# Kernel optimization log

Measured on AMD Instinct MI355X. Metric: run time of the kernel, lower is better.

The kernel has to match this reference:

```python
import jax, jax.numpy as jnp
import numpy as np

DIM = 96
NUM_HEADS = 3
WIN = 7  # window_size (square)


def _relative_position_index(wh, ww):
    coords = np.stack(np.meshgrid(np.arange(wh), np.arange(ww), indexing='ij'))  # [2, wh, ww]
    flat = coords.reshape(2, -1)  # [2, n]
    rel = flat[:, :, None] - flat[:, None, :]  # [2, n, n]
    rel = rel.transpose(1, 2, 0).astype(np.int64)
    rel[..., 0] += wh - 1
    rel[..., 1] += ww - 1
    rel[..., 0] *= 2 * ww - 1
    return rel.sum(-1)  # [n, n]


def setup_inputs() -> dict:
    key = jax.random.key(0)
    ks = jax.random.split(key, 9)
    b, n, c = 8192, WIN * WIN, DIM
    std = 0.02
    inp = {
        'x': jax.random.normal(ks[0], (b, n, c), jnp.float32),
        'v': jax.random.normal(ks[1], (b, n, c), jnp.float32),
        'w_q': jax.random.normal(ks[2], (c, c), jnp.float32) * std,
        'b_q': jnp.zeros((c,), jnp.float32),
        'w_kv': jax.random.normal(ks[3], (c, 2 * c), jnp.float32) * std,
        'b_kv': jnp.zeros((2 * c,), jnp.float32),
        'w_proj': jax.random.normal(ks[4], (c, c), jnp.float32) * std,
        'b_proj': jnp.zeros((c,), jnp.float32),
        'rpb_table': jax.random.normal(ks[5], ((2 * WIN - 1) * (2 * WIN - 1), NUM_HEADS), jnp.float32) * std,
        'rel_index': jnp.asarray(_relative_position_index(WIN, WIN), jnp.int32),
    }
    return inp


def reference(x, v, w_q, b_q, w_kv, b_kv, w_proj, b_proj, rpb_table, rel_index):
    b, n, c = x.shape
    h = NUM_HEADS
    hd = c // h
    scale = hd ** -0.5
    # q: [b, h, n, hd]
    q = (x @ w_q + b_q).reshape(b, n, h, hd).transpose(0, 2, 1, 3) * scale
    kv = (v @ w_kv + b_kv).reshape(b, n, 2, h, hd)
    k = kv[:, :, 0].transpose(0, 2, 1, 3)  # [b, h, n, hd]
    vv = kv[:, :, 1].transpose(0, 2, 1, 3)
    attn = jnp.einsum('bhqd,bhkd->bhqk', q, k)  # [b, h, n, n]
    bias = rpb_table[rel_index.reshape(-1)].reshape(n, n, h).transpose(2, 0, 1)  # [h, n, n]
    attn = jax.nn.softmax(attn + bias[None], axis=-1)
    out = jnp.einsum('bhqk,bhkd->bhqd', attn, vv).transpose(0, 2, 1, 3).reshape(b, n, c)
    return out @ w_proj + b_proj
```

## Files before the change

### kernel.cpp

```cpp
#include <hip/hip_runtime.h>
#include <hip/hip_bf16.h>

typedef __bf16 bf16x8 __attribute__((ext_vector_type(8)));
typedef float f32x4 __attribute__((ext_vector_type(4)));
typedef short s16x8 __attribute__((ext_vector_type(8)));
typedef short s16x4 __attribute__((ext_vector_type(4)));

#define NTOK 49
#define CDIM 96
#define XS_S 104
#define VT_S 72
#define PW_S 72

__device__ __forceinline__ unsigned short f2bf(float f) {
  __hip_bfloat16 h = __float2bfloat16(f);
  return __builtin_bit_cast(unsigned short, h);
}

__global__ void prep(const float* __restrict__ wq, const float* __restrict__ wkv,
                     const float* __restrict__ wproj, const float* __restrict__ rpb,
                     const int* __restrict__ relidx, unsigned short* __restrict__ wsT,
                     float* __restrict__ biasf) {
  const int total = 36864 + 3 * 49 * 64;
  for (int i = blockIdx.x * 256 + threadIdx.x; i < total; i += gridDim.x * 256) {
    if (i < 9216) {
      int oc = i / 96, ic = i - oc * 96;
      wsT[i] = f2bf(wq[ic * 96 + oc]);
    } else if (i < 27648) {
      int j = i - 9216; int oc = j / 96, ic = j - oc * 96;
      wsT[i] = f2bf(wkv[ic * 192 + oc]);
    } else if (i < 36864) {
      int j = i - 27648; int oc = j / 96, ic = j - oc * 96;
      wsT[i] = f2bf(wproj[ic * 96 + oc]);
    } else {
      int j = i - 36864; int h = j / 3136; int rc = j - h * 3136;
      int r = rc >> 6, c = rc & 63;
      biasf[j] = (c < 49) ? rpb[relidx[r * 49 + c] * 3 + h] : 0.f;
    }
  }
}

__launch_bounds__(256, 3)
__global__ void attn_fused(const float* __restrict__ xg, const float* __restrict__ vg,
                           const float* __restrict__ bq, const float* __restrict__ bkv,
                           const float* __restrict__ bproj,
                           const unsigned short* __restrict__ wsT,
                           const float* __restrict__ biasf,
                           float* __restrict__ outg) {
  __shared__ __align__(16) unsigned char smem[53664];
  unsigned short* Qs = (unsigned short*)(smem);
  unsigned short* Ks = (unsigned short*)(smem + 10240);
  unsigned short* Pw = (unsigned short*)(smem + 20432);
  unsigned short* XV = (unsigned short*)(smem + 29648);
  unsigned short* Vs = (unsigned short*)(smem + 43472);

  const int tid = threadIdx.x;
  const int lane = tid & 63;
  const int wv = tid >> 6;
  const int c16 = lane & 15;
  const int g4 = lane >> 4;
  const int win = blockIdx.x;
  const float* xw = xg + (size_t)win * (NTOK * CDIM);
  const float* vw = vg + (size_t)win * (NTOK * CDIM);
  const int MST[4] = {0, 16, 32, 33};

  for (int i = tid; i < 2 * 1176; i += 256) {
    int which = i >= 1176;
    int j = which ? i - 1176 : i;
    int r = j / 24, c4 = (j - r * 24) * 4;
    const float* src = which ? vw : xw;
    float4 f = *(const float4*)(src + r * 96 + c4);
    s16x4 p;
    p[0] = (short)f2bf(f.x); p[1] = (short)f2bf(f.y);
    p[2] = (short)f2bf(f.z); p[3] = (short)f2bf(f.w);
    *(s16x4*)((which ? Vs : XV) + r * XS_S + c4) = p;
  }
  __syncthreads();

  bf16x8 axf[4][3];
#pragma unroll
  for (int m = 0; m < 4; ++m)
#pragma unroll
    for (int k = 0; k < 3; ++k)
      axf[m][k] = *(const bf16x8*)(XV + (MST[m] + c16) * XS_S + k * 32 + g4 * 8);
  __syncthreads();

  unsigned short* VVT = XV;

  const float scale = 0.17677669529663687f;
  for (int nt = wv; nt < 18; nt += 4) {
    f32x4 acc[4] = {{0,0,0,0},{0,0,0,0},{0,0,0,0},{0,0,0,0}};
    const bool isq = nt < 6;
    const unsigned short* wbase = isq ? wsT : wsT + 9216;
    const int ocl = (isq ? nt * 16 : (nt - 6) * 16) + c16;
#pragma unroll
    for (int k = 0; k < 3; ++k) {
      bf16x8 b = *(const bf16x8*)(wbase + ocl * 96 + k * 32 + g4 * 8);
      if (isq) {
#pragma unroll
        for (int m = 0; m < 4; ++m)
          acc[m] = __builtin_amdgcn_mfma_f32_16x16x32_bf16(axf[m][k], b, acc[m], 0, 0, 0);
      } else {
#pragma unroll
        for (int m = 0; m < 4; ++m) {
          bf16x8 av = *(const bf16x8*)(Vs + (MST[m] + c16) * XS_S + k * 32 + g4 * 8);
          acc[m] = __builtin_amdgcn_mfma_f32_16x16x32_bf16(av, b, acc[m], 0, 0, 0);
        }
      }
    }
    if (isq) {
      float bias = bq[ocl];
#pragma unroll
      for (int m = 0; m < 4; ++m) {
        int rb = MST[m] + g4 * 4;
#pragma unroll
        for (int r = 0; r < 4; ++r)
          Qs[(rb + r) * XS_S + ocl] = f2bf((acc[m][r] + bias) * scale);
      }
    } else if (nt < 12) {
      float bias = bkv[ocl];
#pragma unroll
      for (int m = 0; m < 4; ++m) {
        int rb = MST[m] + g4 * 4;
#pragma unroll
        for (int r = 0; r < 4; ++r)
          Ks[(rb + r) * XS_S + ocl] = f2bf(acc[m][r] + bias);
      }
    } else {
      float bias = bkv[ocl];
      int dim = ocl - 96;
#pragma unroll
      for (int m = 0; m < 4; ++m) {
        int rb = MST[m] + g4 * 4;
        if (m < 3) {
          s16x4 p;
#pragma unroll
          for (int r = 0; r < 4; ++r) p[r] = (short)f2bf(acc[m][r] + bias);
          *(s16x4*)(VVT + dim * VT_S + rb) = p;
        } else {
#pragma unroll
          for (int r = 0; r < 4; ++r)
            VVT[dim * VT_S + rb + r] = f2bf(acc[m][r] + bias);
        }
      }
    }
  }
  __syncthreads();

  const int q0 = MST[wv];
  unsigned short* mypw = Pw + wv * 16 * PW_S;
  unsigned short* OUTs = Vs;

  s16x8 vmask;
#pragma unroll
  for (int j = 0; j < 8; ++j)
    vmask[j] = (short)(((32 + g4 * 8 + j) < 49) ? 0xFFFF : 0x0000);

  for (int h = 0; h < 3; ++h) {
    bf16x8 bqf = *(const bf16x8*)(Qs + (q0 + c16) * XS_S + h * 32 + g4 * 8);
    f32x4 s[4];
#pragma unroll
    for (int kt = 0; kt < 4; ++kt) {
      bf16x8 ak = *(const bf16x8*)(Ks + (16 * kt + c16) * XS_S + h * 32 + g4 * 8);
      s[kt] = __builtin_amdgcn_mfma_f32_16x16x32_bf16(ak, bqf, (f32x4){0,0,0,0}, 0, 0, 0);
    }
    const int q = q0 + c16;
    const float* brow = biasf + (h * 49 + q) * 64 + 4 * g4;
    float vals[16];
    float mx = -1e30f;
#pragma unroll
    for (int kt = 0; kt < 4; ++kt) {
      f32x4 bv = *(const f32x4*)(brow + 16 * kt);
#pragma unroll
      for (int r = 0; r < 4; ++r) {
        int key = 16 * kt + 4 * g4 + r;
        float vl = (kt < 3 || key < 49) ? (s[kt][r] + bv[r]) : -1e30f;
        vals[kt * 4 + r] = vl;
        mx = fmaxf(mx, vl);
      }
    }
    mx = fmaxf(mx, __shfl_xor(mx, 16, 64));
    mx = fmaxf(mx, __shfl_xor(mx, 32, 64));
    float sum = 0.f;
#pragma unroll
    for (int j = 0; j < 16; ++j) { vals[j] = __expf(vals[j] - mx); sum += vals[j]; }
    sum += __shfl_xor(sum, 16, 64);
    sum += __shfl_xor(sum, 32, 64);
    float rinv = 1.0f / sum;
#pragma unroll
    for (int kt = 0; kt < 4; ++kt) {
      s16x4 p;
#pragma unroll
      for (int r = 0; r < 4; ++r) p[r] = (short)f2bf(vals[kt * 4 + r] * rinv);
      *(s16x4*)(mypw + c16 * PW_S + 16 * kt + 4 * g4) = p;
    }
    asm volatile("s_waitcnt lgkmcnt(0)" ::: "memory");
    bf16x8 ap0 = *(const bf16x8*)(mypw + c16 * PW_S + g4 * 8);
    bf16x8 ap1 = *(const bf16x8*)(mypw + c16 * PW_S + 32 + g4 * 8);
#pragma unroll
    for (int dt = 0; dt < 2; ++dt) {
      int dim = h * 32 + dt * 16 + c16;
      bf16x8 bv0 = *(const bf16x8*)(VVT + dim * VT_S + g4 * 8);
      s16x8 b1 = *(const s16x8*)(VVT + dim * VT_S + 32 + g4 * 8);
      b1 &= vmask;
      f32x4 o = __builtin_amdgcn_mfma_f32_16x16x32_bf16(ap0, bv0, (f32x4){0,0,0,0}, 0, 0, 0);
      o = __builtin_amdgcn_mfma_f32_16x16x32_bf16(ap1, __builtin_bit_cast(bf16x8, b1), o, 0, 0, 0);
#pragma unroll
      for (int r = 0; r < 4; ++r)
        OUTs[(q0 + 4 * g4 + r) * XS_S + dim] = f2bf(o[r]);
    }
  }
  __syncthreads();

  {
    const int nstart = MST[wv];
    bf16x8 bo[3];
#pragma unroll
    for (int k = 0; k < 3; ++k)
      bo[k] = *(const bf16x8*)(OUTs + (nstart + c16) * XS_S + k * 32 + g4 * 8);
    const unsigned short* wp = wsT + 27648;
    const bool store_ok = (wv < 3) || (c16 == 15);
    const int token = nstart + c16;
    float* orow = outg + (size_t)win * (NTOK * CDIM) + token * 96;
#pragma unroll
    for (int mt = 0; mt < 6; ++mt) {
      f32x4 acc = {0, 0, 0, 0};
      int mrow = mt * 16 + c16;
#pragma unroll
      for (int k = 0; k < 3; ++k) {
        bf16x8 a = *(const bf16x8*)(wp + mrow * 96 + k * 32 + g4 * 8);
        acc = __builtin_amdgcn_mfma_f32_16x16x32_bf16(a, bo[k], acc, 0, 0, 0);
      }
      int oc0 = mt * 16 + g4 * 4;
      if (store_ok) {
        float4 bb = *(const float4*)(bproj + oc0);
        float4 o4;
        o4.x = acc[0] + bb.x; o4.y = acc[1] + bb.y;
        o4.z = acc[2] + bb.z; o4.w = acc[3] + bb.w;
        *(float4*)(orow + oc0) = o4;
      }
    }
  }
}

extern "C" void kernel_launch(void* const* d_in, const int* in_sizes, int n_in,
                              void* d_out, int out_size, void* d_ws, size_t ws_size,
                              hipStream_t stream) {
  const float* x     = (const float*)d_in[0];
  const float* v     = (const float*)d_in[1];
  const float* wq    = (const float*)d_in[2];
  const float* bq    = (const float*)d_in[3];
  const float* wkv   = (const float*)d_in[4];
  const float* bkv   = (const float*)d_in[5];
  const float* wproj = (const float*)d_in[6];
  const float* bproj = (const float*)d_in[7];
  const float* rpb   = (const float*)d_in[8];
  const int*   relidx= (const int*)d_in[9];
  float* out = (float*)d_out;
  unsigned short* wsT = (unsigned short*)d_ws;
  float* biasf = (float*)((char*)d_ws + 73728);
  int nwin = in_sizes[0] / (NTOK * CDIM);

  hipLaunchKernelGGL(prep, dim3(181), dim3(256), 0, stream,
                     wq, wkv, wproj, rpb, relidx, wsT, biasf);
  hipLaunchKernelGGL(attn_fused, dim3(nwin), dim3(256), 0, stream,
                     x, v, bq, bkv, bproj, wsT, biasf, out);
}
```

Baseline: 277.0 us.

## Load x/v directly to registers, fuse proj per head, shrink LDS for occupancy

Each wave now loads its own 16 token rows of x and v straight from global memory into bf16 MFMA fragments, so the LDS staging copy and two barriers go away. The Q projection stays per wave in a private buffer, and only K and V-transposed are shared. The output projection is accumulated per head inside the attention loop, so the block-wide OUTs buffer and the final barrier are no longer needed. LDS drops from about 53.7KB to 37.3KB and launch bounds rise to 4 blocks per CU. In exchange, each wave computes full-width weight tiles and rereads all 18 weight tiles from global memory, and the 6 extra accumulators raise register pressure.

```diff
diff --git a/kernel.cpp b/kernel.cpp
--- a/kernel.cpp
+++ b/kernel.cpp
@@ -8,13 +8,24 @@
 
 #define NTOK 49
 #define CDIM 96
-#define XS_S 104
+#define KS_S 104
 #define VT_S 72
-#define PW_S 72
+#define BN_S 104
 
 __device__ __forceinline__ unsigned short f2bf(float f) {
   __hip_bfloat16 h = __float2bfloat16(f);
   return __builtin_bit_cast(unsigned short, h);
+}
+
+__device__ __forceinline__ bf16x8 ld_cvt8(const float* p) {
+  float4 a = *(const float4*)p;
+  float4 b = *(const float4*)(p + 4);
+  s16x8 r;
+  r[0] = (short)f2bf(a.x); r[1] = (short)f2bf(a.y);
+  r[2] = (short)f2bf(a.z); r[3] = (short)f2bf(a.w);
+  r[4] = (short)f2bf(b.x); r[5] = (short)f2bf(b.y);
+  r[6] = (short)f2bf(b.z); r[7] = (short)f2bf(b.w);
+  return __builtin_bit_cast(bf16x8, r);
 }
 
 __global__ void prep(const float* __restrict__ wq, const float* __restrict__ wkv,
@@ -40,19 +51,16 @@
   }
 }
 
-__launch_bounds__(256, 3)
+__launch_bounds__(256, 4)
 __global__ void attn_fused(const float* __restrict__ xg, const float* __restrict__ vg,
                            const float* __restrict__ bq, const float* __restrict__ bkv,
                            const float* __restrict__ bproj,
                            const unsigned short* __restrict__ wsT,
                            const float* __restrict__ biasf,
                            float* __restrict__ outg) {
-  __shared__ __align__(16) unsigned char smem[53664];
-  unsigned short* Qs = (unsigned short*)(smem);
-  unsigned short* Ks = (unsigned short*)(smem + 10240);
-  unsigned short* Pw = (unsigned short*)(smem + 20432);
-  unsigned short* XV = (unsigned short*)(smem + 29648);
-  unsigned short* Vs = (unsigned short*)(smem + 43472);
+  __shared__ __align__(16) unsigned char smem[37328];
+  unsigned short* Ks  = (unsigned short*)smem;
+  unsigned short* VVT = (unsigned short*)(smem + 10192);
 
   const int tid = threadIdx.x;
   const int lane = tid & 63;
@@ -60,109 +68,83 @@
   const int c16 = lane & 15;
   const int g4 = lane >> 4;
   const int win = blockIdx.x;
-  const float* xw = xg + (size_t)win * (NTOK * CDIM);
-  const float* vw = vg + (size_t)win * (NTOK * CDIM);
-  const int MST[4] = {0, 16, 32, 33};
-
-  for (int i = tid; i < 2 * 1176; i += 256) {
-    int which = i >= 1176;
-    int j = which ? i - 1176 : i;
-    int r = j / 24, c4 = (j - r * 24) * 4;
-    const float* src = which ? vw : xw;
-    float4 f = *(const float4*)(src + r * 96 + c4);
-    s16x4 p;
-    p[0] = (short)f2bf(f.x); p[1] = (short)f2bf(f.y);
-    p[2] = (short)f2bf(f.z); p[3] = (short)f2bf(f.w);
-    *(s16x4*)((which ? Vs : XV) + r * XS_S + c4) = p;
+  const int q0 = (wv == 0) ? 0 : (wv == 1) ? 16 : (wv == 2) ? 32 : 33;
+  unsigned short* bnc = (unsigned short*)(smem + 24016) + wv * (16 * BN_S);
+
+  const float* xrow = xg + (size_t)win * (NTOK * CDIM) + (q0 + c16) * CDIM;
+  const float* vrow = vg + (size_t)win * (NTOK * CDIM) + (q0 + c16) * CDIM;
+
+  bf16x8 xf[3];
+#pragma unroll
+  for (int k = 0; k < 3; ++k) xf[k] = ld_cvt8(xrow + k * 32 + g4 * 8);
+  const float scale = 0.17677669529663687f;
+#pragma unroll
+  for (int nt = 0; nt < 6; ++nt) {
+    f32x4 acc = {0, 0, 0, 0};
+    const int ocl = nt * 16 + c16;
+#pragma unroll
+    for (int k = 0; k < 3; ++k) {
+      bf16x8 b = *(const bf16x8*)(wsT + ocl * 96 + k * 32 + g4 * 8);
+      acc = __builtin_amdgcn_mfma_f32_16x16x32_bf16(xf[k], b, acc, 0, 0, 0);
+    }
+    float bias = bq[ocl];
+#pragma unroll
+    for (int r = 0; r < 4; ++r)
+      bnc[(4 * g4 + r) * BN_S + ocl] = f2bf((acc[r] + bias) * scale);
+  }
+
+  bf16x8 vf[3];
+#pragma unroll
+  for (int k = 0; k < 3; ++k) vf[k] = ld_cvt8(vrow + k * 32 + g4 * 8);
+#pragma unroll
+  for (int nt = 0; nt < 12; ++nt) {
+    f32x4 acc = {0, 0, 0, 0};
+    const int ocl = nt * 16 + c16;
+#pragma unroll
+    for (int k = 0; k < 3; ++k) {
+      bf16x8 b = *(const bf16x8*)(wsT + 9216 + ocl * 96 + k * 32 + g4 * 8);
+      acc = __builtin_amdgcn_mfma_f32_16x16x32_bf16(vf[k], b, acc, 0, 0, 0);
+    }
+    float bias = bkv[ocl];
+    if (nt < 6) {
+#pragma unroll
+      for (int r = 0; r < 4; ++r)
+        Ks[(q0 + 4 * g4 + r) * KS_S + ocl] = f2bf(acc[r] + bias);
+    } else {
+      int dim = ocl - 96;
+      int rb = q0 + 4 * g4;
+      if (wv < 3) {
+        s16x4 p;
+#pragma unroll
+        for (int r = 0; r < 4; ++r) p[r] = (short)f2bf(acc[r] + bias);
+        *(s16x4*)(VVT + dim * VT_S + rb) = p;
+      } else {
+#pragma unroll
+        for (int r = 0; r < 4; ++r)
+          VVT[dim * VT_S + rb + r] = f2bf(acc[r] + bias);
+      }
+    }
   }
   __syncthreads();
 
-  bf16x8 axf[4][3];
-#pragma unroll
-  for (int m = 0; m < 4; ++m)
-#pragma unroll
-    for (int k = 0; k < 3; ++k)
-      axf[m][k] = *(const bf16x8*)(XV + (MST[m] + c16) * XS_S + k * 32 + g4 * 8);
-  __syncthreads();
-
-  unsigned short* VVT = XV;
-
-  const float scale = 0.17677669529663687f;
-  for (int nt = wv; nt < 18; nt += 4) {
-    f32x4 acc[4] = {{0,0,0,0},{0,0,0,0},{0,0,0,0},{0,0,0,0}};
-    const bool isq = nt < 6;
-    const unsigned short* wbase = isq ? wsT : wsT + 9216;
-    const int ocl = (isq ? nt * 16 : (nt - 6) * 16) + c16;
-#pragma unroll
-    for (int k = 0; k < 3; ++k) {
-      bf16x8 b = *(const bf16x8*)(wbase + ocl * 96 + k * 32 + g4 * 8);
-      if (isq) {
-#pragma unroll
-        for (int m = 0; m < 4; ++m)
-          acc[m] = __builtin_amdgcn_mfma_f32_16x16x32_bf16(axf[m][k], b, acc[m], 0, 0, 0);
-      } else {
-#pragma unroll
-        for (int m = 0; m < 4; ++m) {
-          bf16x8 av = *(const bf16x8*)(Vs + (MST[m] + c16) * XS_S + k * 32 + g4 * 8);
-          acc[m] = __builtin_amdgcn_mfma_f32_16x16x32_bf16(av, b, acc[m], 0, 0, 0);
-        }
-      }
-    }
-    if (isq) {
-      float bias = bq[ocl];
-#pragma unroll
-      for (int m = 0; m < 4; ++m) {
-        int rb = MST[m] + g4 * 4;
-#pragma unroll
-        for (int r = 0; r < 4; ++r)
-          Qs[(rb + r) * XS_S + ocl] = f2bf((acc[m][r] + bias) * scale);
-      }
-    } else if (nt < 12) {
-      float bias = bkv[ocl];
-#pragma unroll
-      for (int m = 0; m < 4; ++m) {
-        int rb = MST[m] + g4 * 4;
-#pragma unroll
-        for (int r = 0; r < 4; ++r)
-          Ks[(rb + r) * XS_S + ocl] = f2bf(acc[m][r] + bias);
-      }
-    } else {
-      float bias = bkv[ocl];
-      int dim = ocl - 96;
-#pragma unroll
-      for (int m = 0; m < 4; ++m) {
-        int rb = MST[m] + g4 * 4;
-        if (m < 3) {
-          s16x4 p;
-#pragma unroll
-          for (int r = 0; r < 4; ++r) p[r] = (short)f2bf(acc[m][r] + bias);
-          *(s16x4*)(VVT + dim * VT_S + rb) = p;
-        } else {
-#pragma unroll
-          for (int r = 0; r < 4; ++r)
-            VVT[dim * VT_S + rb + r] = f2bf(acc[m][r] + bias);
-        }
-      }
-    }
-  }
-  __syncthreads();
-
-  const int q0 = MST[wv];
-  unsigned short* mypw = Pw + wv * 16 * PW_S;
-  unsigned short* OUTs = Vs;
+  bf16x8 qf[3];
+#pragma unroll
+  for (int h = 0; h < 3; ++h)
+    qf[h] = *(const bf16x8*)(bnc + c16 * BN_S + h * 32 + g4 * 8);
 
   s16x8 vmask;
 #pragma unroll
   for (int j = 0; j < 8; ++j)
     vmask[j] = (short)(((32 + g4 * 8 + j) < 49) ? 0xFFFF : 0x0000);
 
+  f32x4 oacc[6] = {{0,0,0,0},{0,0,0,0},{0,0,0,0},{0,0,0,0},{0,0,0,0},{0,0,0,0}};
+
   for (int h = 0; h < 3; ++h) {
-    bf16x8 bqf = *(const bf16x8*)(Qs + (q0 + c16) * XS_S + h * 32 + g4 * 8);
     f32x4 s[4];
 #pragma unroll
     for (int kt = 0; kt < 4; ++kt) {
-      bf16x8 ak = *(const bf16x8*)(Ks + (16 * kt + c16) * XS_S + h * 32 + g4 * 8);
-      s[kt] = __builtin_amdgcn_mfma_f32_16x16x32_bf16(ak, bqf, (f32x4){0,0,0,0}, 0, 0, 0);
+      bf16x8 ak = *(const bf16x8*)(Ks + (16 * kt + c16) * KS_S + h * 32 + g4 * 8);
+      s[kt] = __builtin_amdgcn_mfma_f32_16x16x32_bf16(ak, qf[h], (f32x4){0,0,0,0}, 0, 0, 0);
     }
     const int q = q0 + c16;
     const float* brow = biasf + (h * 49 + q) * 64 + 4 * g4;
@@ -192,11 +174,12 @@
       s16x4 p;
 #pragma unroll
       for (int r = 0; r < 4; ++r) p[r] = (short)f2bf(vals[kt * 4 + r] * rinv);
-      *(s16x4*)(mypw + c16 * PW_S + 16 * kt + 4 * g4) = p;
+      *(s16x4*)(bnc + c16 * BN_S + 16 * kt + 4 * g4) = p;
     }
     asm volatile("s_waitcnt lgkmcnt(0)" ::: "memory");
-    bf16x8 ap0 = *(const bf16x8*)(mypw + c16 * PW_S + g4 * 8);
-    bf16x8 ap1 = *(const bf16x8*)(mypw + c16 * PW_S + 32 + g4 * 8);
+    __builtin_amdgcn_sched_barrier(0);
+    bf16x8 ap0 = *(const bf16x8*)(bnc + c16 * BN_S + g4 * 8);
+    bf16x8 ap1 = *(const bf16x8*)(bnc + c16 * BN_S + 32 + g4 * 8);
 #pragma unroll
     for (int dt = 0; dt < 2; ++dt) {
       int dim = h * 32 + dt * 16 + c16;
@@ -207,36 +190,32 @@
       o = __builtin_amdgcn_mfma_f32_16x16x32_bf16(ap1, __builtin_bit_cast(bf16x8, b1), o, 0, 0, 0);
 #pragma unroll
       for (int r = 0; r < 4; ++r)
-        OUTs[(q0 + 4 * g4 + r) * XS_S + dim] = f2bf(o[r]);
-    }
-  }
-  __syncthreads();
+        bnc[(4 * g4 + r) * BN_S + dt * 16 + c16] = f2bf(o[r]);
+    }
+    asm volatile("s_waitcnt lgkmcnt(0)" ::: "memory");
+    __builtin_amdgcn_sched_barrier(0);
+    bf16x8 bo = *(const bf16x8*)(bnc + c16 * BN_S + g4 * 8);
+#pragma unroll
+    for (int mt = 0; mt < 6; ++mt) {
+      bf16x8 a = *(const bf16x8*)(wsT + 27648 + (mt * 16 + c16) * 96 + h * 32 + g4 * 8);
+      oacc[mt] = __builtin_amdgcn_mfma_f32_16x16x32_bf16(a, bo, oacc[mt], 0, 0, 0);
+    }
+    asm volatile("s_waitcnt lgkmcnt(0)" ::: "memory");
+    __builtin_amdgcn_sched_barrier(0);
+  }
 
   {
-    const int nstart = MST[wv];
-    bf16x8 bo[3];
-#pragma unroll
-    for (int k = 0; k < 3; ++k)
-      bo[k] = *(const bf16x8*)(OUTs + (nstart + c16) * XS_S + k * 32 + g4 * 8);
-    const unsigned short* wp = wsT + 27648;
     const bool store_ok = (wv < 3) || (c16 == 15);
-    const int token = nstart + c16;
+    const int token = q0 + c16;
     float* orow = outg + (size_t)win * (NTOK * CDIM) + token * 96;
 #pragma unroll
     for (int mt = 0; mt < 6; ++mt) {
-      f32x4 acc = {0, 0, 0, 0};
-      int mrow = mt * 16 + c16;
-#pragma unroll
-      for (int k = 0; k < 3; ++k) {
-        bf16x8 a = *(const bf16x8*)(wp + mrow * 96 + k * 32 + g4 * 8);
-        acc = __builtin_amdgcn_mfma_f32_16x16x32_bf16(a, bo[k], acc, 0, 0, 0);
-      }
       int oc0 = mt * 16 + g4 * 4;
       if (store_ok) {
         float4 bb = *(const float4*)(bproj + oc0);
         float4 o4;
-        o4.x = acc[0] + bb.x; o4.y = acc[1] + bb.y;
-        o4.z = acc[2] + bb.z; o4.w = acc[3] + bb.w;
+        o4.x = oacc[mt][0] + bb.x; o4.y = oacc[mt][1] + bb.y;
+        o4.z = oacc[mt][2] + bb.z; o4.w = oacc[mt][3] + bb.w;
         *(float4*)(orow + oc0) = o4;
       }
     }
```

After: 258.7 us. 6.6% less time.
